# Kernel tuning notes

Hardware: AMD Instinct MI355X
Metric: run time of the kernel (lower is better)

Reference implementation:

```python
import jax, jax.numpy as jnp
import numpy as np

H = 16
LN_EPS = 1e-5


def setup_inputs() -> dict:
    key = jax.random.key(0)
    ks = jax.random.split(key, 8)
    B, N, D = 2, 2048, 1024
    s = D ** -0.5
    return {
        "q_s": jax.random.normal(ks[0], (B, N, D), jnp.float32),
        "pos_emb": jax.random.normal(ks[1], (B, N, D), jnp.float32),
        "Wq": jax.random.normal(ks[2], (D, D), jnp.float32) * s,
        "Wk": jax.random.normal(ks[3], (D, D), jnp.float32) * s,
        "Wv": jax.random.normal(ks[4], (D, D), jnp.float32) * s,
        "Wo": jax.random.normal(ks[5], (D, D), jnp.float32) * s,
        "bo": jnp.zeros((D,), jnp.float32),
        "ln_g": jnp.ones((D,), jnp.float32),
        "ln_b": jnp.zeros((D,), jnp.float32),
    }


def _split_heads(t):
    b, n, d = t.shape
    return t.reshape(b, n, H, d // H).transpose(0, 2, 1, 3)  # b h n d


def reference(q_s, pos_emb, Wq, Wk, Wv, Wo, bo, ln_g, ln_b):
    # self-attention: k_s = v_s = q_s
    q = _split_heads(q_s @ Wq)
    k = _split_heads(q_s @ Wk)
    v = _split_heads(q_s @ Wv)
    p = _split_heads(pos_emb)
    scale = q.shape[-1] ** -0.5
    # content-content + content-position attention logits: [b,h,i,j]
    att = (jnp.einsum('bhid,bhjd->bhij', q, k) + jnp.einsum('bhid,bhjd->bhij', q, p)) * scale
    att = jax.nn.softmax(att, axis=-1)
    o = jnp.einsum('bhij,bhjd->bhid', att, v)
    b, h, n, d = o.shape
    o = o.transpose(0, 2, 1, 3).reshape(b, n, h * d)
    o = o @ Wo + bo  # out_layer (dropout rate 0 -> identity)
    x = o + q_s  # residual
    mu = jnp.mean(x, axis=-1, keepdims=True)
    var = jnp.var(x, axis=-1, keepdims=True)
    return (x - mu) * jax.lax.rsqrt(var + LN_EPS) * ln_g + ln_b
```

## Files before the change

kernel.cpp:

```cpp
#include <hip/hip_runtime.h>
#include <hip/hip_bf16.h>
#include <stdint.h>

typedef unsigned short u16;
typedef unsigned int u32;
typedef short s16x8 __attribute__((ext_vector_type(8)));
typedef short s16x4 __attribute__((ext_vector_type(4)));
typedef float f32x4 __attribute__((ext_vector_type(4)));

#define MFMA(a, b, c) __builtin_amdgcn_mfma_f32_16x16x32_bf16((a), (b), (c), 0, 0, 0)

__device__ __forceinline__ u16 f2bf_rte(float f) {
  __hip_bfloat16 h = __float2bfloat16(f);
  u16 u;
  __builtin_memcpy(&u, &h, 2);
  return u;
}

__device__ __forceinline__ void gload16(const u16* g, u16* l) {
  __builtin_amdgcn_global_load_lds((const __attribute__((address_space(1))) u32*)g,
                                   (__attribute__((address_space(3))) u32*)l, 16, 0, 0);
}

__global__ __launch_bounds__(256) void k_cvt(const float* __restrict__ in,
                                             u16* __restrict__ out, int n8) {
  int i = blockIdx.x * 256 + threadIdx.x;
  if (i >= n8) return;
  const f32x4* p = (const f32x4*)(in + (size_t)i * 8);
  f32x4 a = p[0], b = p[1];
  s16x8 o;
  for (int k = 0; k < 4; ++k) o[k] = (short)f2bf_rte(a[k]);
  for (int k = 0; k < 4; ++k) o[4 + k] = (short)f2bf_rte(b[k]);
  *(s16x8*)(out + (size_t)i * 8) = o;
}

__global__ __launch_bounds__(256) void k_transpose_w(const float* __restrict__ W0,
                                                     const float* __restrict__ W1,
                                                     const float* __restrict__ W2,
                                                     const float* __restrict__ W3,
                                                     u16* __restrict__ out) {
  const int z = blockIdx.z;
  const float* in = (z == 0) ? W0 : (z == 1) ? W1 : (z == 2) ? W2 : W3;
  u16* o = out + (size_t)z * 1024 * 1024;
  __shared__ u16 tile[64][65];
  const int t = threadIdx.x, tx = t & 63, ty = t >> 6;
  const int r0 = blockIdx.y * 64, c0 = blockIdx.x * 64;
  for (int rr = 0; rr < 16; ++rr) {
    int row = rr * 4 + ty;
    tile[row][tx] = f2bf_rte(in[(size_t)(r0 + row) * 1024 + c0 + tx]);
  }
  __syncthreads();
  for (int rr = 0; rr < 16; ++rr) {
    int row = rr * 4 + ty;
    o[(size_t)(c0 + row) * 1024 + r0 + tx] = tile[tx][row];
  }
}

__global__ __launch_bounds__(256) void k_transpose_v(const u16* __restrict__ V,
                                                     u16* __restrict__ Vt) {
  __shared__ u16 tile[64][65];
  const int t = threadIdx.x, tx = t & 63, ty = t >> 6;
  const int j0 = blockIdx.x * 64;
  const int bh = blockIdx.y;
  const u16* src = V + (size_t)bh * 2048 * 64;
  u16* dst = Vt + (size_t)bh * 64 * 2048;
  for (int rr = 0; rr < 16; ++rr) {
    int row = rr * 4 + ty;
    tile[row][tx] = src[(size_t)(j0 + row) * 64 + tx];
  }
  __syncthreads();
  for (int rr = 0; rr < 16; ++rr) {
    int d = rr * 4 + ty;
    dst[(size_t)d * 2048 + j0 + tx] = tile[tx][d];
  }
}

__global__ __launch_bounds__(256) void k_qkv_gemm(const u16* __restrict__ X,
                                                  const u16* __restrict__ WT,
                                                  const float* __restrict__ pos,
                                                  u16* __restrict__ Qh,
                                                  u16* __restrict__ Kh,
                                                  u16* __restrict__ Vh) {
  __shared__ u16 As[3][4096];
  __shared__ u16 Bs[3][4096];
  const int t = threadIdx.x;
  const int lane = t & 63, wid = t >> 6;
  const int wr = wid >> 1, wc = wid & 1;
  const int g = lane >> 4, lr = lane & 15;
  const int lin = blockIdx.y * 24 + blockIdx.x;
  const int swz = (lin & 7) * 96 + (lin >> 3);
  const int m0 = (swz / 24) * 128, n0 = (swz % 24) * 128;

  const int srcRow = t >> 2;
  const int srcKsw = ((t & 3) * 8) ^ (((t >> 3) & 3) << 3);
  const u16* aSrc = &X[(size_t)(m0 + srcRow) * 1024 + srcKsw];
  const u16* bSrc = &WT[(size_t)(n0 + srcRow) * 1024 + srcKsw];

  const int csw = (g * 8) ^ (((lr >> 1) & 3) << 3);

  f32x4 acc[4][4] = {};

#define QKV_STAGE(buf, k0)                                   \
  {                                                          \
    gload16(aSrc + (k0), &As[buf][wid * 512]);               \
    gload16(aSrc + 65536 + (k0), &As[buf][wid * 512 + 2048]);\
    gload16(bSrc + (k0), &Bs[buf][wid * 512]);               \
    gload16(bSrc + 65536 + (k0), &Bs[buf][wid * 512 + 2048]);\
  }

  QKV_STAGE(0, 0);
  QKV_STAGE(1, 32);
  QKV_STAGE(2, 64);
  for (int k = 0; k < 32; ++k) {
    if (k < 30) {
      asm volatile("s_waitcnt vmcnt(8)" ::: "memory");
    } else if (k == 30) {
      asm volatile("s_waitcnt vmcnt(4)" ::: "memory");
    } else {
      asm volatile("s_waitcnt vmcnt(0)" ::: "memory");
    }
    __builtin_amdgcn_sched_barrier(0);
    __builtin_amdgcn_s_barrier();
    const int cur = k % 3;
    s16x8 a[4], b[4];
#pragma unroll
    for (int mi = 0; mi < 4; ++mi)
      a[mi] = *(const s16x8*)&As[cur][(wr * 64 + mi * 16 + lr) * 32 + csw];
#pragma unroll
    for (int nj = 0; nj < 4; ++nj)
      b[nj] = *(const s16x8*)&Bs[cur][(wc * 64 + nj * 16 + lr) * 32 + csw];
#pragma unroll
    for (int mi = 0; mi < 4; ++mi)
#pragma unroll
      for (int nj = 0; nj < 4; ++nj)
        acc[mi][nj] = MFMA(a[mi], b[nj], acc[mi][nj]);
    __builtin_amdgcn_s_barrier();
    if (k < 29) QKV_STAGE(cur, (k + 3) * 32);
  }
#undef QKV_STAGE

  const float QSCALE = 0.125f * 1.44269504f;
  for (int mi = 0; mi < 4; ++mi) {
    for (int nj = 0; nj < 4; ++nj) {
      const int n_g = n0 + wc * 64 + nj * 16 + lr;
      const int buf = n_g >> 10;
      const int col = n_g & 1023;
      const int h = col >> 6, d = col & 63;
      u16* dst = (buf == 0) ? Qh : ((buf == 1) ? Kh : Vh);
      for (int r = 0; r < 4; ++r) {
        const int row = m0 + wr * 64 + mi * 16 + g * 4 + r;
        const int b = row >> 11, n = row & 2047;
        float v = acc[mi][nj][r];
        if (buf == 1) v += pos[(size_t)row * 1024 + col];
        if (buf == 0) v *= QSCALE;
        dst[(size_t)((b * 16 + h) * 2048 + n) * 64 + d] = f2bf_rte(v);
      }
    }
  }
}

__global__ __launch_bounds__(512, 4) void k_attn(const u16* __restrict__ Qh,
                                                 const u16* __restrict__ Kh,
                                                 const u16* __restrict__ Vt,
                                                 u16* __restrict__ Oh) {
  const int t = threadIdx.x, lane = t & 63, wid = t >> 6;
  const int g = lane >> 4, lr = lane & 15;
  const int hid = blockIdx.x;
  const int lid = (hid & 7) * 64 + (hid >> 3);
  const int bh = lid >> 4, itile = lid & 15;
  const int i0 = itile * 128 + wid * 16;

  __shared__ char Ks[2][8192];
  __shared__ char Vs[2][8192];

  const u16* Qp = Qh + (size_t)bh * 2048 * 64;
  const u16* Kp = Kh + (size_t)bh * 2048 * 64;
  const u16* Vp = Vt + (size_t)bh * 64 * 2048;

  s16x8 aq[2];
  aq[0] = *(const s16x8*)&Qp[(size_t)(i0 + lr) * 64 + g * 8];
  aq[1] = *(const s16x8*)&Qp[(size_t)(i0 + lr) * 64 + 32 + g * 8];

  f32x4 oa[4] = {};
  float ms = -1e30f, ls = 0.f;

  const int srow = t >> 3;
  const int sch = (t & 7) * 16;
  const int swz = (srow & 7) << 4;
  const int sb = (srow * 128 + sch) ^ swz;
  const u16* kB = &Kp[(size_t)srow * 64 + (sch >> 1)];
  const u16* vB = &Vp[(size_t)srow * 2048 + (sch >> 1)];

  s16x8 kr = *(const s16x8*)kB;
  s16x8 vr = *(const s16x8*)vB;
  *(s16x8*)(Ks[0] + sb) = kr;
  *(s16x8*)(Vs[0] + sb) = vr;
  __syncthreads();

  for (int tt = 0; tt < 32; ++tt) {
    const int cur = tt & 1;
    if (tt < 31) {
      const size_t j1 = (size_t)(tt + 1) * 64;
      kr = *(const s16x8*)(kB + j1 * 64);
      vr = *(const s16x8*)(vB + j1);
    }
    const char* Kc = Ks[cur];
    const char* Vc = Vs[cur];

    f32x4 s[4] = {};
    __builtin_amdgcn_s_setprio(1);
#pragma unroll
    for (int jf = 0; jf < 4; ++jf) {
      const int row = jf * 16 + lr;
      const int bw = (row & 7) << 4;
      s16x8 bk0 = *(const s16x8*)(Kc + ((row * 128 + g * 16) ^ bw));
      s16x8 bk1 = *(const s16x8*)(Kc + ((row * 128 + 64 + g * 16) ^ bw));
      s[jf] = MFMA(bk0, aq[0], s[jf]);
      s[jf] = MFMA(bk1, aq[1], s[jf]);
    }
    __builtin_amdgcn_s_setprio(0);

    float tl = s[0][0];
#pragma unroll
    for (int jf = 0; jf < 4; ++jf)
#pragma unroll
      for (int r = 0; r < 4; ++r)
        if (jf | r) tl = fmaxf(tl, s[jf][r]);
    if (!__all(tl <= ms + 8.f)) {
      float tm = fmaxf(tl, __shfl_xor(tl, 16, 64));
      tm = fmaxf(tm, __shfl_xor(tm, 32, 64));
      float mn = fmaxf(ms, tm);
      float al = __builtin_amdgcn_exp2f(ms - mn);
      ls *= al;
      ms = mn;
#pragma unroll
      for (int r = 0; r < 4; ++r) {
        float ab = __shfl(al, g * 4 + r, 64);
#pragma unroll
        for (int df = 0; df < 4; ++df) oa[df][r] *= ab;
      }
    }

#pragma unroll
    for (int jf = 0; jf < 4; ++jf)
#pragma unroll
      for (int r = 0; r < 4; ++r) {
        float p = __builtin_amdgcn_exp2f(s[jf][r] - ms);
        s[jf][r] = p;
        ls += p;
      }

    u32 pk[4][2];
#pragma unroll
    for (int jf = 0; jf < 4; ++jf) {
      asm("v_cvt_pk_bf16_f32 %0, %1, %2" : "=v"(pk[jf][0]) : "v"(s[jf][0]), "v"(s[jf][1]));
      asm("v_cvt_pk_bf16_f32 %0, %1, %2" : "=v"(pk[jf][1]) : "v"(s[jf][2]), "v"(s[jf][3]));
    }

    s16x8 pa[2];
#pragma unroll
    for (int c = 0; c < 2; ++c) {
      u32 w_[4];
#pragma unroll
      for (int wl = 0; wl < 2; ++wl) {
        u32 A = pk[2 * c][wl], B = pk[2 * c + 1][wl];
        asm("v_permlane32_swap_b32 %0, %1" : "+v"(A), "+v"(B));
        asm("v_permlane16_swap_b32 %0, %1" : "+v"(A), "+v"(B));
        w_[wl] = A;
        w_[2 + wl] = B;
      }
      __builtin_memcpy(&pa[c], w_, 16);
    }

    __builtin_amdgcn_s_setprio(1);
#pragma unroll
    for (int df = 0; df < 4; ++df) {
      const int row = df * 16 + lr;
      const int bw = (row & 7) << 4;
      s16x8 bv0 = *(const s16x8*)(Vc + ((row * 128 + g * 16) ^ bw));
      s16x8 bv1 = *(const s16x8*)(Vc + ((row * 128 + 64 + g * 16) ^ bw));
      oa[df] = MFMA(pa[0], bv0, oa[df]);
      oa[df] = MFMA(pa[1], bv1, oa[df]);
    }
    __builtin_amdgcn_s_setprio(0);

    if (tt < 31) {
      *(s16x8*)(Ks[cur ^ 1] + sb) = kr;
      *(s16x8*)(Vs[cur ^ 1] + sb) = vr;
    }
    __syncthreads();
  }

  ls += __shfl_xor(ls, 16, 64);
  ls += __shfl_xor(ls, 32, 64);
  float lb[4];
#pragma unroll
  for (int r = 0; r < 4; ++r) lb[r] = __shfl(ls, g * 4 + r, 64);

  u16* Op = Oh + (size_t)bh * 2048 * 64;
#pragma unroll
  for (int df = 0; df < 4; ++df)
#pragma unroll
    for (int r = 0; r < 4; ++r) {
      const int row0 = i0 + g * 4 + r;
      Op[(size_t)row0 * 64 + df * 16 + lr] = f2bf_rte(oa[df][r] / lb[r]);
    }
}

__global__ __launch_bounds__(256) void k_out_gemm(const u16* __restrict__ Oh,
                                                  const u16* __restrict__ WTo,
                                                  const float* __restrict__ bo,
                                                  const float* __restrict__ qs,
                                                  float* __restrict__ X) {
  __shared__ u16 As[3][4096];
  __shared__ u16 Bs[3][4096];
  const int t = threadIdx.x;
  const int lane = t & 63, wid = t >> 6;
  const int wr = wid >> 1, wc = wid & 1;
  const int g = lane >> 4, lr = lane & 15;
  const int lin = blockIdx.y * 8 + blockIdx.x;
  const int swz = (lin & 7) * 32 + (lin >> 3);
  const int m0 = (swz / 8) * 128, n0 = (swz % 8) * 128;

  const int srcRow = t >> 2;
  const int srcKsw = ((t & 3) * 8) ^ (((t >> 3) & 3) << 3);
  const int rg = m0 + srcRow, bb0 = rg >> 11, nn0 = rg & 2047;
  const int rg2 = rg + 64, bb2 = rg2 >> 11, nn2 = rg2 & 2047;
  const u16* bSrc = &WTo[(size_t)(n0 + srcRow) * 1024 + srcKsw];
  const int csw = (g * 8) ^ (((lr >> 1) & 3) << 3);

  f32x4 acc[4][4] = {};

#define OUT_STAGE(buf, k0)                                                        \
  {                                                                               \
    const int h_ = (k0) >> 6, d_ = ((k0) & 63) + srcKsw;                          \
    gload16(&Oh[((size_t)(bb0 * 16 + h_) * 2048 + nn0) * 64 + d_],                \
            &As[buf][wid * 512]);                                                 \
    gload16(&Oh[((size_t)(bb2 * 16 + h_) * 2048 + nn2) * 64 + d_],                \
            &As[buf][wid * 512 + 2048]);                                          \
    gload16(bSrc + (k0), &Bs[buf][wid * 512]);                                    \
    gload16(bSrc + 65536 + (k0), &Bs[buf][wid * 512 + 2048]);                     \
  }

  OUT_STAGE(0, 0);
  OUT_STAGE(1, 32);
  OUT_STAGE(2, 64);
  for (int k = 0; k < 32; ++k) {
    if (k < 30) {
      asm volatile("s_waitcnt vmcnt(8)" ::: "memory");
    } else if (k == 30) {
      asm volatile("s_waitcnt vmcnt(4)" ::: "memory");
    } else {
      asm volatile("s_waitcnt vmcnt(0)" ::: "memory");
    }
    __builtin_amdgcn_sched_barrier(0);
    __builtin_amdgcn_s_barrier();
    const int cur = k % 3;
    s16x8 a[4], b[4];
#pragma unroll
    for (int mi = 0; mi < 4; ++mi)
      a[mi] = *(const s16x8*)&As[cur][(wr * 64 + mi * 16 + lr) * 32 + csw];
#pragma unroll
    for (int nj = 0; nj < 4; ++nj)
      b[nj] = *(const s16x8*)&Bs[cur][(wc * 64 + nj * 16 + lr) * 32 + csw];
#pragma unroll
    for (int mi = 0; mi < 4; ++mi)
#pragma unroll
      for (int nj = 0; nj < 4; ++nj)
        acc[mi][nj] = MFMA(a[mi], b[nj], acc[mi][nj]);
    __builtin_amdgcn_s_barrier();
    if (k < 29) OUT_STAGE(cur, (k + 3) * 32);
  }
#undef OUT_STAGE

  for (int mi = 0; mi < 4; ++mi) {
    for (int nj = 0; nj < 4; ++nj) {
      const int col = n0 + wc * 64 + nj * 16 + lr;
      for (int r = 0; r < 4; ++r) {
        const int row = m0 + wr * 64 + mi * 16 + g * 4 + r;
        float v = acc[mi][nj][r] + bo[col] + qs[(size_t)row * 1024 + col];
        X[(size_t)row * 1024 + col] = v;
      }
    }
  }
}

__global__ __launch_bounds__(256) void k_ln(const float* __restrict__ X,
                                            const float* __restrict__ gg,
                                            const float* __restrict__ bb,
                                            float* __restrict__ out) {
  const int row = blockIdx.x, t = threadIdx.x;
  const int wid = t >> 6, lane = t & 63;
  const float* xr = X + (size_t)row * 1024;
  f32x4 x = *(const f32x4*)&xr[t * 4];
  float s1 = x[0] + x[1] + x[2] + x[3];
  float s2 = x[0] * x[0] + x[1] * x[1] + x[2] * x[2] + x[3] * x[3];
  for (int off = 32; off > 0; off >>= 1) {
    s1 += __shfl_down(s1, off, 64);
    s2 += __shfl_down(s2, off, 64);
  }
  __shared__ float red[2][4];
  if (lane == 0) { red[0][wid] = s1; red[1][wid] = s2; }
  __syncthreads();
  s1 = red[0][0] + red[0][1] + red[0][2] + red[0][3];
  s2 = red[1][0] + red[1][1] + red[1][2] + red[1][3];
  const float mu = s1 * (1.f / 1024.f);
  const float var = s2 * (1.f / 1024.f) - mu * mu;
  const float rstd = rsqrtf(var + 1e-5f);
  f32x4 gv = *(const f32x4*)&gg[t * 4];
  f32x4 bv = *(const f32x4*)&bb[t * 4];
  f32x4 ov;
  for (int i = 0; i < 4; ++i) ov[i] = (x[i] - mu) * rstd * gv[i] + bv[i];
  *(f32x4*)&out[(size_t)row * 1024 + t * 4] = ov;
}

extern "C" void kernel_launch(void* const* d_in, const int* in_sizes, int n_in,
                              void* d_out, int out_size, void* d_ws, size_t ws_size,
                              hipStream_t stream) {
  (void)in_sizes; (void)n_in; (void)out_size; (void)ws_size;
  const float* q_s = (const float*)d_in[0];
  const float* pos = (const float*)d_in[1];
  const float* Wq = (const float*)d_in[2];
  const float* Wk = (const float*)d_in[3];
  const float* Wv = (const float*)d_in[4];
  const float* Wo = (const float*)d_in[5];
  const float* bo = (const float*)d_in[6];
  const float* lng = (const float*)d_in[7];
  const float* lnb = (const float*)d_in[8];
  float* out = (float*)d_out;

  u16* ws = (u16*)d_ws;
  const size_t MB1 = 1024 * 1024;
  u16* WT  = ws;
  u16* Xbf = ws + 4 * MB1;
  u16* Qh  = Xbf + 4 * MB1;
  u16* Kh  = Qh + 4 * MB1;
  u16* Vh  = Kh + 4 * MB1;
  u16* Vt  = Vh + 4 * MB1;
  u16* Oh  = Vt + 4 * MB1;
  float* Xb = (float*)Qh;

  dim3 blk(256);
  k_cvt<<<dim3(2048), blk, 0, stream>>>(q_s, Xbf, 4 * MB1 / 8);
  k_transpose_w<<<dim3(16, 16, 4), blk, 0, stream>>>(Wq, Wk, Wv, Wo, WT);
  k_qkv_gemm<<<dim3(24, 32), blk, 0, stream>>>(Xbf, WT, pos, Qh, Kh, Vh);
  k_transpose_v<<<dim3(32, 32), blk, 0, stream>>>(Vh, Vt);
  k_attn<<<dim3(512), dim3(512), 0, stream>>>(Qh, Kh, Vt, Oh);
  k_out_gemm<<<dim3(8, 32), blk, 0, stream>>>(Oh, WT + 3 * MB1, bo, q_s, Xb);
  k_ln<<<4096, blk, 0, stream>>>(Xb, lng, lnb, out);
}
```

Measured before the change: 142.9 us.

## Use 4-stage direct-to-LDS K/V pipeline in attention kernel

Replaces the register-staged double-buffered K/V tile loads with global_load_lds direct-to-LDS copies into a 4-deep ring buffer, issuing tiles three iterations ahead. Explicit vmcnt waits and one barrier per iteration replace the register round-trip and end-of-loop syncthreads. The goal is deeper latency hiding and lower VGPR pressure. The cost is 64KB of LDS per block, which may lower occupancy against the launch bound of 4 blocks. The swizzle is now applied on the global address side, and correctness relies on the vmcnt counts and the single barrier guarding buffer reuse.

New measurement: 144.3 us. No clear change (+1.0%).

```diff
diff --git a/kernel.cpp b/kernel.cpp
--- a/kernel.cpp
+++ b/kernel.cpp
@@ -170,8 +170,8 @@
   const int bh = lid >> 4, itile = lid & 15;
   const int i0 = itile * 128 + wid * 16;
 
-  __shared__ char Ks[2][8192];
-  __shared__ char Vs[2][8192];
+  __shared__ char Ks[4][8192];
+  __shared__ char Vs[4][8192];
 
   const u16* Qp = Qh + (size_t)bh * 2048 * 64;
   const u16* Kp = Kh + (size_t)bh * 2048 * 64;
@@ -186,26 +186,34 @@
 
   const int srow = t >> 3;
   const int sch = (t & 7) * 16;
-  const int swz = (srow & 7) << 4;
-  const int sb = (srow * 128 + sch) ^ swz;
-  const u16* kB = &Kp[(size_t)srow * 64 + (sch >> 1)];
-  const u16* vB = &Vp[(size_t)srow * 2048 + (sch >> 1)];
-
-  s16x8 kr = *(const s16x8*)kB;
-  s16x8 vr = *(const s16x8*)vB;
-  *(s16x8*)(Ks[0] + sb) = kr;
-  *(s16x8*)(Vs[0] + sb) = vr;
-  __syncthreads();
+  const int schS = sch ^ ((srow & 7) << 4);
+  const u16* kB = &Kp[(size_t)srow * 64 + (schS >> 1)];
+  const u16* vB = &Vp[(size_t)srow * 2048 + (schS >> 1)];
+
+#define ATTN_STAGE(p)                                          \
+  {                                                            \
+    gload16(kB + (size_t)(p) * 4096, (u16*)Ks[(p) & 3] + wid * 512); \
+    gload16(vB + (size_t)(p) * 64, (u16*)Vs[(p) & 3] + wid * 512);   \
+  }
+
+  ATTN_STAGE(0);
+  ATTN_STAGE(1);
+  ATTN_STAGE(2);
 
   for (int tt = 0; tt < 32; ++tt) {
-    const int cur = tt & 1;
-    if (tt < 31) {
-      const size_t j1 = (size_t)(tt + 1) * 64;
-      kr = *(const s16x8*)(kB + j1 * 64);
-      vr = *(const s16x8*)(vB + j1);
-    }
-    const char* Kc = Ks[cur];
-    const char* Vc = Vs[cur];
+    if (tt < 30) {
+      asm volatile("s_waitcnt vmcnt(4)" ::: "memory");
+    } else if (tt == 30) {
+      asm volatile("s_waitcnt vmcnt(2)" ::: "memory");
+    } else {
+      asm volatile("s_waitcnt vmcnt(0)" ::: "memory");
+    }
+    __builtin_amdgcn_sched_barrier(0);
+    __builtin_amdgcn_s_barrier();
+    if (tt < 29) ATTN_STAGE(tt + 3);
+
+    const char* Kc = Ks[tt & 3];
+    const char* Vc = Vs[tt & 3];
 
     f32x4 s[4] = {};
     __builtin_amdgcn_s_setprio(1);
@@ -283,13 +291,8 @@
       oa[df] = MFMA(pa[1], bv1, oa[df]);
     }
     __builtin_amdgcn_s_setprio(0);
-
-    if (tt < 31) {
-      *(s16x8*)(Ks[cur ^ 1] + sb) = kr;
-      *(s16x8*)(Vs[cur ^ 1] + sb) = vr;
-    }
-    __syncthreads();
-  }
+  }
+#undef ATTN_STAGE
 
   ls += __shfl_xor(ls, 16, 64);
   ls += __shfl_xor(ls, 32, 64);
```
